# Kernel tuning notes

Hardware: AMD Instinct MI355X
Metric: run time of the kernel (lower is better)

The kernel has to match this reference:

```python
import jax, jax.numpy as jnp
import numpy as np

EMBED_DIM = 1024
NUM_HEADS = 16
D_K = EMBED_DIM // NUM_HEADS
BATCH, SEQ = 4, 2048


def setup_inputs() -> dict:
    key = jax.random.key(0)
    ks = jax.random.split(key, 6)
    s = 1.0 / np.sqrt(EMBED_DIM)
    return {
        "x": jax.random.normal(ks[0], (BATCH, SEQ, EMBED_DIM), dtype=jnp.float32),
        "mask": jnp.ones((BATCH, SEQ), dtype=jnp.int32),
        "Wq": jax.random.uniform(ks[1], (EMBED_DIM, EMBED_DIM), jnp.float32, -s, s),
        "Wk": jax.random.uniform(ks[2], (EMBED_DIM, EMBED_DIM), jnp.float32, -s, s),
        "Wv": jax.random.uniform(ks[3], (EMBED_DIM, EMBED_DIM), jnp.float32, -s, s),
        "Wo": jax.random.uniform(ks[4], (EMBED_DIM, EMBED_DIM), jnp.float32, -s, s),
    }


def reference(x, mask, Wq, Wk, Wv, Wo):
    B, S, E = x.shape
    H, Dk = NUM_HEADS, D_K
    # nn.Linear: y = x @ W.T ; reshape to [B, H, S, Dk]
    def proj(W):
        return jnp.einsum('bse,fe->bsf', x, W).reshape(B, S, H, Dk).transpose(0, 2, 1, 3)
    q, k, v = proj(Wq), proj(Wk), proj(Wv)
    scores = jnp.einsum('bhqd,bhkd->bhqk', q, k) / jnp.sqrt(jnp.float32(Dk))
    # key-padding mask: [B, S] -> [B, 1, 1, S]; 0 means masked with -inf
    scores = jnp.where(mask[:, None, None, :] == 0, -jnp.inf, scores)
    attn = jax.nn.softmax(scores, axis=-1)  # dropout is identity (p=0 / eval)
    out = jnp.einsum('bhqk,bhkd->bhqd', attn, v)
    out = out.transpose(0, 2, 1, 3).reshape(B, S, E)
    return jnp.einsum('bse,fe->bsf', out, Wo)
```

## Files before the change

kernel.cpp:

```cpp
#include <hip/hip_runtime.h>

typedef __attribute__((ext_vector_type(8))) __bf16   bf16x8;
typedef __attribute__((ext_vector_type(8))) _Float16 f16x8;
typedef __attribute__((ext_vector_type(2))) __fp16   h16x2;
typedef __attribute__((ext_vector_type(8))) __fp16   h16x8;
typedef __attribute__((ext_vector_type(4))) float    f32x4;

#define MFMA_BF16 __builtin_amdgcn_mfma_f32_16x16x32_bf16
#define MFMA_F16  __builtin_amdgcn_mfma_f32_16x16x32_f16

__global__ __launch_bounds__(256)
void prep_all(const float* __restrict__ x,  const float* __restrict__ Wq,
              const float* __restrict__ Wk, const float* __restrict__ Wv,
              const float* __restrict__ Wo, const int* __restrict__ mask,
              __bf16* __restrict__ xh, __bf16* __restrict__ w3,
              __bf16* __restrict__ wo, float* __restrict__ bias)
{
    const int i = blockIdx.x * 256 + threadIdx.x;
    const int WSZ8 = 131072;

    if (i < 1572864) {
        const float* src; __bf16* dst; int o8;
        if (i < 1048576)      { src = x;  dst = xh;            o8 = i; }
        else if (i < 1179648) { src = Wq; dst = w3;            o8 = i - 1048576; }
        else if (i < 1310720) { src = Wk; dst = w3 + 1048576;  o8 = i - 1179648; }
        else if (i < 1441792) { src = Wv; dst = w3 + 2097152;  o8 = i - 1310720; }
        else                  { src = Wo; dst = wo;            o8 = i - 1441792; }
        float4 v0 = *(const float4*)(src + (size_t)o8 * 8);
        float4 v1 = *(const float4*)(src + (size_t)o8 * 8 + 4);
        float xs[8] = {v0.x, v0.y, v0.z, v0.w, v1.x, v1.y, v1.z, v1.w};
        bf16x8 h8;
        #pragma unroll
        for (int jj = 0; jj < 8; jj++) h8[jj] = (__bf16)xs[jj];
        *(bf16x8*)(dst + (size_t)o8 * 8) = h8;
    } else {
        int c = i - 1572864;
        int4 m0 = *(const int4*)(mask + c * 8);
        int4 m1 = *(const int4*)(mask + c * 8 + 4);
        float4 b0, b1;
        b0.x = m0.x ? 0.f : -30000.f;  b0.y = m0.y ? 0.f : -30000.f;
        b0.z = m0.z ? 0.f : -30000.f;  b0.w = m0.w ? 0.f : -30000.f;
        b1.x = m1.x ? 0.f : -30000.f;  b1.y = m1.y ? 0.f : -30000.f;
        b1.z = m1.z ? 0.f : -30000.f;  b1.w = m1.w ? 0.f : -30000.f;
        *(float4*)(bias + c * 8)     = b0;
        *(float4*)(bias + c * 8 + 4) = b1;
    }
}

#define GEMM_DECLS                                                          \
    __shared__ __bf16 Ah[128][40], Bh[128][40];                             \
    const int t    = threadIdx.x;                                           \
    const int lane = t & 63;                                                \
    const int wid  = t >> 6;                                                \
    const int l15  = lane & 15;                                             \
    const int lg   = lane >> 4;                                             \
    const int wr   = wid >> 1, wc = wid & 1;

#define GEMM_LOOP(Ag, Bg, m0, brow0, K)                                     \
    f32x4 acc[4][4];                                                        \
    _Pragma("unroll")                                                       \
    for (int i = 0; i < 4; i++)                                             \
        _Pragma("unroll")                                                   \
        for (int jj = 0; jj < 4; jj++)                                      \
            _Pragma("unroll")                                               \
            for (int r = 0; r < 4; r++) acc[i][jj][r] = 0.f;                \
    for (int k0 = 0; k0 < K; k0 += 32) {                                    \
        __syncthreads();                                                    \
        _Pragma("unroll")                                                   \
        for (int i = 0; i < 2; i++) {                                       \
            int id = t + 256 * i;                                           \
            int row = id >> 2, cc = id & 3;                                 \
            *(bf16x8*)&Ah[row][cc*8] =                                      \
                *(const bf16x8*)(Ag + (size_t)(m0 + row) * K + k0 + cc*8);  \
            *(bf16x8*)&Bh[row][cc*8] =                                      \
                *(const bf16x8*)(Bg + (size_t)(brow0 + row) * K + k0 + cc*8);\
        }                                                                   \
        __syncthreads();                                                    \
        bf16x8 ah[4];                                                       \
        _Pragma("unroll")                                                   \
        for (int mr = 0; mr < 4; mr++)                                      \
            ah[mr] = *(const bf16x8*)&Ah[wr*64 + mr*16 + l15][lg*8];        \
        _Pragma("unroll")                                                   \
        for (int nr = 0; nr < 4; nr++) {                                    \
            bf16x8 bh = *(const bf16x8*)&Bh[wc*64 + nr*16 + l15][lg*8];     \
            _Pragma("unroll")                                               \
            for (int mr = 0; mr < 4; mr++)                                  \
                acc[mr][nr] = MFMA_BF16(ah[mr], bh, acc[mr][nr], 0, 0, 0);  \
        }                                                                   \
    }

__global__ __launch_bounds__(256, 4)
void gemm_qkv(const __bf16* __restrict__ xh, const __bf16* __restrict__ w3,
              __bf16* __restrict__ qh, __bf16* __restrict__ kh,
              _Float16* __restrict__ vh)
{
    GEMM_DECLS
    const int K = 1024, N = 1024;
    const int m0     = blockIdx.x * 128;
    const int by     = blockIdx.y;
    const int region = by >> 3;
    const int n0     = (by & 7) * 128;
    const int brow0  = region * 1024 + n0;
    GEMM_LOOP(xh, w3, m0, brow0, K)

    constexpr float QSCALE = 0.18033688011112f;
    #pragma unroll
    for (int mr = 0; mr < 4; mr++)
    #pragma unroll
    for (int r = 0; r < 4; r++) {
        int row = m0 + wr*64 + mr*16 + lg*4 + r;
        #pragma unroll
        for (int nr = 0; nr < 4; nr++) {
            int col = n0 + wc*64 + nr*16 + l15;
            size_t off = (size_t)row * N + col;
            float v = acc[mr][nr][r];
            if (region == 0)      qh[off] = (__bf16)(v * QSCALE);
            else if (region == 1) kh[off] = (__bf16)v;
            else                  vh[off] = (_Float16)v;
        }
    }
}

__global__ __launch_bounds__(256, 4)
void gemm_out(const __bf16* __restrict__ aoh, const __bf16* __restrict__ woh,
              float* __restrict__ out, int M, int N, int K)
{
    GEMM_DECLS
    const int m0 = blockIdx.x * 128, n0 = blockIdx.y * 128;
    GEMM_LOOP(aoh, woh, m0, n0, K)

    #pragma unroll
    for (int mr = 0; mr < 4; mr++)
    #pragma unroll
    for (int r = 0; r < 4; r++) {
        int row = m0 + wr*64 + mr*16 + lg*4 + r;
        #pragma unroll
        for (int nr = 0; nr < 4; nr++) {
            int col = n0 + wc*64 + nr*16 + l15;
            out[(size_t)row * N + col] = acc[mr][nr][r];
        }
    }
}

__global__ __launch_bounds__(512, 2)
void attn_bf16(const __bf16* __restrict__ Qg, const __bf16* __restrict__ Kg,
               const _Float16* __restrict__ Vg, const float* __restrict__ biasg,
               __bf16* AO)
{
    const int S = 2048, E = 1024;
    __shared__ __align__(16) char smem[36864];

    const int tid  = threadIdx.x;
    const int lane = tid & 63;
    const int wid  = tid >> 6;
    const int l15  = lane & 15;
    const int lg   = lane >> 4;

    const int fid = blockIdx.x;
    const int xcd = fid & 7;
    const int j   = fid >> 3;
    const int bh  = xcd * 8 + (j >> 3);
    const int qb  = j & 7;
    const int h   = bh & 15;
    const int b   = bh >> 4;
    const int q0  = qb * 256;
    const size_t base = (size_t)b * S * E + (size_t)h * 64;

    bf16x8 qf[2][2];
    #pragma unroll
    for (int mg = 0; mg < 2; mg++) {
        size_t qoff = base + (size_t)(q0 + wid*32 + mg*16 + l15) * E;
        #pragma unroll
        for (int kc = 0; kc < 2; kc++)
            qf[mg][kc] = *(const bf16x8*)(Qg + qoff + kc*32 + lg*8);
    }

    f32x4 o[2][4], osum[2];
    #pragma unroll
    for (int mg = 0; mg < 2; mg++) {
        #pragma unroll
        for (int nt = 0; nt < 4; nt++)
            #pragma unroll
            for (int r = 0; r < 4; r++) o[mg][nt][r] = 0.f;
        #pragma unroll
        for (int r = 0; r < 4; r++) osum[mg][r] = 0.f;
    }

    f16x8 ones8;
    #pragma unroll
    for (int jj = 0; jj < 8; jj++) ones8[jj] = (_Float16)1.0f;

    const int srow = tid >> 3;
    const int scc  = tid & 7;
    const int sg   = ((srow & 12) >> 2) * 8 + ((srow >> 4) & 1) * 4
                   + (srow & 3) + (srow & 32);

    bf16x8 kpre; f16x8 vpre;
    {
        size_t g0 = base + (size_t)srow * E + scc * 8;
        kpre = *(const bf16x8*)(Kg + g0);
        vpre = *(const f16x8*)(Vg + g0);
    }

    const int NT = S / 64;
    for (int t = 0; t < NT; t++) {
        const int k0 = t * 64;
        char* buf = smem + (t & 1) * 18432;
        __bf16   (*Kh)[72] = (__bf16 (*)[72])buf;
        _Float16 (*Vt)[72] = (_Float16 (*)[72])(buf + 9216);

        *(bf16x8*)&Kh[srow][scc*8] = kpre;
        {
            int colw = (((sg >> 3) ^ scc) << 3) + (sg & 7);
            #pragma unroll
            for (int jj = 0; jj < 8; jj++)
                Vt[scc*8 + jj][colw] = vpre[jj];
        }

        if (t + 1 < NT) {
            size_t gn = base + (size_t)(k0 + 64 + srow) * E + scc * 8;
            kpre = *(const bf16x8*)(Kg + gn);
            vpre = *(const f16x8*)(Vg + gn);
        }
        __syncthreads();

        f32x4 sf[2][4];
        #pragma unroll
        for (int kvb = 0; kvb < 4; kvb++) {
            f32x4 bias4 = *(const f32x4*)(biasg + b * S + k0 + kvb*16 + lg*4);
            sf[0][kvb] = bias4;
            sf[1][kvb] = bias4;
        }
        #pragma unroll
        for (int kc = 0; kc < 2; kc++)
            #pragma unroll
            for (int kvb = 0; kvb < 4; kvb++) {
                bf16x8 kb = *(const bf16x8*)&Kh[kvb*16 + l15][kc*32 + lg*8];
                #pragma unroll
                for (int mg = 0; mg < 2; mg++)
                    sf[mg][kvb] = MFMA_BF16(kb, qf[mg][kc], sf[mg][kvb], 0, 0, 0);
            }

        f16x8 pa[2][2];
        #pragma unroll
        for (int mg = 0; mg < 2; mg++) {
            float p[4][4];
            #pragma unroll
            for (int kvb = 0; kvb < 4; kvb++)
                #pragma unroll
                for (int r = 0; r < 4; r++)
                    p[kvb][r] = __builtin_amdgcn_exp2f(sf[mg][kvb][r]);
            #pragma unroll
            for (int hh = 0; hh < 2; hh++) {
                h16x2 c0 = __builtin_amdgcn_cvt_pkrtz(p[2*hh][0],   p[2*hh][1]);
                h16x2 c1 = __builtin_amdgcn_cvt_pkrtz(p[2*hh][2],   p[2*hh][3]);
                h16x2 c2 = __builtin_amdgcn_cvt_pkrtz(p[2*hh+1][0], p[2*hh+1][1]);
                h16x2 c3 = __builtin_amdgcn_cvt_pkrtz(p[2*hh+1][2], p[2*hh+1][3]);
                h16x8 t8 = __builtin_shufflevector(
                    __builtin_shufflevector(c0, c1, 0, 1, 2, 3),
                    __builtin_shufflevector(c2, c3, 0, 1, 2, 3),
                    0, 1, 2, 3, 4, 5, 6, 7);
                pa[mg][hh] = __builtin_bit_cast(f16x8, t8);
            }
        }

        #pragma unroll
        for (int hh = 0; hh < 2; hh++) {
            #pragma unroll
            for (int nt = 0; nt < 4; nt++) {
                int c8p = (hh*4 + lg) ^ (nt*2 + (l15 >> 3));
                f16x8 vb = *(const f16x8*)&Vt[nt*16 + l15][c8p*8];
                o[0][nt] = MFMA_F16(pa[0][hh], vb, o[0][nt], 0, 0, 0);
                o[1][nt] = MFMA_F16(pa[1][hh], vb, o[1][nt], 0, 0, 0);
            }
            osum[0] = MFMA_F16(pa[0][hh], ones8, osum[0], 0, 0, 0);
            osum[1] = MFMA_F16(pa[1][hh], ones8, osum[1], 0, 0, 0);
        }
    }

    float inv[2][4];
    #pragma unroll
    for (int mg = 0; mg < 2; mg++)
        #pragma unroll
        for (int r = 0; r < 4; r++) inv[mg][r] = 1.0f / osum[mg][r];

    unsigned short* Pu = (unsigned short*)smem;
    __syncthreads();
    #pragma unroll
    for (int mg = 0; mg < 2; mg++)
        #pragma unroll
        for (int r = 0; r < 4; r++)
            #pragma unroll
            for (int nt = 0; nt < 4; nt++) {
                __bf16 v = (__bf16)(o[mg][nt][r] * inv[mg][r]);
                Pu[(wid*32 + mg*16 + lg*4 + r) * 72 + nt*16 + l15] =
                    *(unsigned short*)&v;
            }
    __syncthreads();
    #pragma unroll
    for (int i = 0; i < 4; i++) {
        int u   = tid + 512 * i;
        int row = u >> 3, c8 = u & 7;
        bf16x8 v8;
        #pragma unroll
        for (int jj = 0; jj < 8; jj++) {
            unsigned short us = Pu[row * 72 + c8*8 + jj];
            v8[jj] = *(__bf16*)&us;
        }
        *(bf16x8*)(AO + base + (size_t)(q0 + row) * E + c8 * 8) = v8;
    }
}

extern "C" void kernel_launch(void* const* d_in, const int* in_sizes, int n_in,
                              void* d_out, int out_size, void* d_ws, size_t ws_size,
                              hipStream_t stream)
{
    const float* x    = (const float*)d_in[0];
    const int*   mask = (const int*)  d_in[1];
    const float* Wq   = (const float*)d_in[2];
    const float* Wk   = (const float*)d_in[3];
    const float* Wv   = (const float*)d_in[4];
    const float* Wo   = (const float*)d_in[5];
    float* out = (float*)d_out;

    const int B = 4, S = 2048, E = 1024;
    const int M = B * S;
    const size_t SZ  = (size_t)M * E;
    const size_t WSZ = (size_t)E * E;
    const size_t PB  = SZ * sizeof(__bf16);

    char* ws = (char*)d_ws;
    __bf16*   qh = (__bf16*)(ws);
    __bf16*   kh = (__bf16*)(ws + PB);
    _Float16* vh = (_Float16*)(ws + 2*PB);
    __bf16*   xh = (__bf16*)(ws + 3*PB);
    __bf16*   w3 = (__bf16*)(ws + 4*PB);
    __bf16*   wo = (__bf16*)(ws + 4*PB + 3*WSZ*sizeof(__bf16));
    float*    bs = (float*)(ws + 4*PB + 4*WSZ*sizeof(__bf16));

    prep_all<<<dim3(6148), dim3(256), 0, stream>>>(
        x, Wq, Wk, Wv, Wo, mask, xh, w3, wo, bs);

    gemm_qkv<<<dim3(M/128, 24), dim3(256), 0, stream>>>(xh, w3, qh, kh, vh);

    attn_bf16<<<dim3(512), dim3(512), 0, stream>>>(qh, kh, vh, bs, qh);

    gemm_out<<<dim3(M/128, E/128), dim3(256), 0, stream>>>(qh, wo, out, M, E, E);
}
```

Before: 196.6 us.

## Software-pipeline attention PV with next QK and halve block size

The attention kernel now runs 256-thread blocks over 128-query tiles, launching twice as many blocks, and each thread stages two K/V rows per tile. The main loop is software-pipelined: the PV MFMAs for the previous tile, using the retained probabilities and the previous V buffer, are issued alongside the QK MFMAs of the current tile, with a prologue and an epilogue. The aim is to overlap exp and convert latency with MFMA work and to improve occupancy and load balance. In exchange, each block reloads K/V for fewer queries, which doubles K/V traffic, adds an extra barrier per iteration, and raises register pressure.

```diff
diff --git a/kernel.cpp b/kernel.cpp
--- a/kernel.cpp
+++ b/kernel.cpp
@@ -17,7 +17,6 @@
               __bf16* __restrict__ wo, float* __restrict__ bias)
 {
     const int i = blockIdx.x * 256 + threadIdx.x;
-    const int WSZ8 = 131072;
 
     if (i < 1572864) {
         const float* src; __bf16* dst; int o8;
@@ -142,7 +141,7 @@
     }
 }
 
-__global__ __launch_bounds__(512, 2)
+__global__ __launch_bounds__(256, 2)
 void attn_bf16(const __bf16* __restrict__ Qg, const __bf16* __restrict__ Kg,
                const _Float16* __restrict__ Vg, const float* __restrict__ biasg,
                __bf16* AO)
@@ -159,11 +158,11 @@
     const int fid = blockIdx.x;
     const int xcd = fid & 7;
     const int j   = fid >> 3;
-    const int bh  = xcd * 8 + (j >> 3);
-    const int qb  = j & 7;
+    const int bh  = xcd * 8 + (j >> 4);
+    const int qb  = j & 15;
     const int h   = bh & 15;
     const int b   = bh >> 4;
-    const int q0  = qb * 256;
+    const int q0  = qb * 128;
     const size_t base = (size_t)b * S * E + (size_t)h * 64;
 
     bf16x8 qf[2][2];
@@ -190,46 +189,49 @@
     #pragma unroll
     for (int jj = 0; jj < 8; jj++) ones8[jj] = (_Float16)1.0f;
 
-    const int srow = tid >> 3;
-    const int scc  = tid & 7;
-    const int sg   = ((srow & 12) >> 2) * 8 + ((srow >> 4) & 1) * 4
-                   + (srow & 3) + (srow & 32);
-
-    bf16x8 kpre; f16x8 vpre;
+    const int srow0 = tid >> 3;
+    const int srow1 = srow0 + 32;
+    const int scc   = tid & 7;
+    const int sg0   = ((srow0 & 12) >> 2) * 8 + ((srow0 >> 4) & 1) * 4
+                    + (srow0 & 3) + (srow0 & 32);
+    const int sg1   = ((srow1 & 12) >> 2) * 8 + ((srow1 >> 4) & 1) * 4
+                    + (srow1 & 3) + (srow1 & 32);
+    const int colw0 = (((sg0 >> 3) ^ scc) << 3) + (sg0 & 7);
+    const int colw1 = (((sg1 >> 3) ^ scc) << 3) + (sg1 & 7);
+
+    bf16x8 kpre0, kpre1; f16x8 vpre0, vpre1;
     {
-        size_t g0 = base + (size_t)srow * E + scc * 8;
-        kpre = *(const bf16x8*)(Kg + g0);
-        vpre = *(const f16x8*)(Vg + g0);
+        size_t ga = base + (size_t)srow0 * E + scc * 8;
+        size_t gb = base + (size_t)srow1 * E + scc * 8;
+        kpre0 = *(const bf16x8*)(Kg + ga);  vpre0 = *(const f16x8*)(Vg + ga);
+        kpre1 = *(const bf16x8*)(Kg + gb);  vpre1 = *(const f16x8*)(Vg + gb);
     }
 
     const int NT = S / 64;
-    for (int t = 0; t < NT; t++) {
-        const int k0 = t * 64;
-        char* buf = smem + (t & 1) * 18432;
-        __bf16   (*Kh)[72] = (__bf16 (*)[72])buf;
-        _Float16 (*Vt)[72] = (_Float16 (*)[72])(buf + 9216);
-
-        *(bf16x8*)&Kh[srow][scc*8] = kpre;
+    f16x8 pa_prev[2][2];
+
+    {
+        __bf16   (*Kh)[72] = (__bf16 (*)[72])smem;
+        _Float16 (*Vt)[72] = (_Float16 (*)[72])(smem + 9216);
+        *(bf16x8*)&Kh[srow0][scc*8] = kpre0;
+        *(bf16x8*)&Kh[srow1][scc*8] = kpre1;
+        #pragma unroll
+        for (int jj = 0; jj < 8; jj++) Vt[scc*8 + jj][colw0] = vpre0[jj];
+        #pragma unroll
+        for (int jj = 0; jj < 8; jj++) Vt[scc*8 + jj][colw1] = vpre1[jj];
         {
-            int colw = (((sg >> 3) ^ scc) << 3) + (sg & 7);
-            #pragma unroll
-            for (int jj = 0; jj < 8; jj++)
-                Vt[scc*8 + jj][colw] = vpre[jj];
-        }
-
-        if (t + 1 < NT) {
-            size_t gn = base + (size_t)(k0 + 64 + srow) * E + scc * 8;
-            kpre = *(const bf16x8*)(Kg + gn);
-            vpre = *(const f16x8*)(Vg + gn);
+            size_t ga = base + (size_t)(64 + srow0) * E + scc * 8;
+            size_t gb = base + (size_t)(64 + srow1) * E + scc * 8;
+            kpre0 = *(const bf16x8*)(Kg + ga);  vpre0 = *(const f16x8*)(Vg + ga);
+            kpre1 = *(const bf16x8*)(Kg + gb);  vpre1 = *(const f16x8*)(Vg + gb);
         }
         __syncthreads();
 
         f32x4 sf[2][4];
         #pragma unroll
         for (int kvb = 0; kvb < 4; kvb++) {
-            f32x4 bias4 = *(const f32x4*)(biasg + b * S + k0 + kvb*16 + lg*4);
-            sf[0][kvb] = bias4;
-            sf[1][kvb] = bias4;
+            f32x4 bias4 = *(const f32x4*)(biasg + b * S + kvb*16 + lg*4);
+            sf[0][kvb] = bias4;  sf[1][kvb] = bias4;
         }
         #pragma unroll
         for (int kc = 0; kc < 2; kc++)
@@ -240,8 +242,6 @@
                 for (int mg = 0; mg < 2; mg++)
                     sf[mg][kvb] = MFMA_BF16(kb, qf[mg][kc], sf[mg][kvb], 0, 0, 0);
             }
-
-        f16x8 pa[2][2];
         #pragma unroll
         for (int mg = 0; mg < 2; mg++) {
             float p[4][4];
@@ -260,21 +260,101 @@
                     __builtin_shufflevector(c0, c1, 0, 1, 2, 3),
                     __builtin_shufflevector(c2, c3, 0, 1, 2, 3),
                     0, 1, 2, 3, 4, 5, 6, 7);
-                pa[mg][hh] = __builtin_bit_cast(f16x8, t8);
-            }
-        }
+                pa_prev[mg][hh] = __builtin_bit_cast(f16x8, t8);
+            }
+        }
+    }
+
+    for (int t = 1; t < NT; t++) {
+        const int k0 = t * 64;
+        char* bufc = smem + (t & 1) * 18432;
+        char* bufp = smem + ((t - 1) & 1) * 18432;
+        __bf16   (*Kh)[72]  = (__bf16 (*)[72])bufc;
+        _Float16 (*Vt)[72]  = (_Float16 (*)[72])(bufc + 9216);
+        _Float16 (*Vtp)[72] = (_Float16 (*)[72])(bufp + 9216);
+
+        __syncthreads();
+        *(bf16x8*)&Kh[srow0][scc*8] = kpre0;
+        *(bf16x8*)&Kh[srow1][scc*8] = kpre1;
+        #pragma unroll
+        for (int jj = 0; jj < 8; jj++) Vt[scc*8 + jj][colw0] = vpre0[jj];
+        #pragma unroll
+        for (int jj = 0; jj < 8; jj++) Vt[scc*8 + jj][colw1] = vpre1[jj];
+
+        if (t + 1 < NT) {
+            size_t ga = base + (size_t)(k0 + 64 + srow0) * E + scc * 8;
+            size_t gb = base + (size_t)(k0 + 64 + srow1) * E + scc * 8;
+            kpre0 = *(const bf16x8*)(Kg + ga);  vpre0 = *(const f16x8*)(Vg + ga);
+            kpre1 = *(const bf16x8*)(Kg + gb);  vpre1 = *(const f16x8*)(Vg + gb);
+        }
+        __syncthreads();
+
+        f32x4 sf[2][4];
+        #pragma unroll
+        for (int kvb = 0; kvb < 4; kvb++) {
+            f32x4 bias4 = *(const f32x4*)(biasg + b * S + k0 + kvb*16 + lg*4);
+            sf[0][kvb] = bias4;  sf[1][kvb] = bias4;
+        }
+        #pragma unroll
+        for (int kc = 0; kc < 2; kc++)
+            #pragma unroll
+            for (int kvb = 0; kvb < 4; kvb++) {
+                bf16x8 kb = *(const bf16x8*)&Kh[kvb*16 + l15][kc*32 + lg*8];
+                #pragma unroll
+                for (int mg = 0; mg < 2; mg++)
+                    sf[mg][kvb] = MFMA_BF16(kb, qf[mg][kc], sf[mg][kvb], 0, 0, 0);
+            }
 
         #pragma unroll
         for (int hh = 0; hh < 2; hh++) {
             #pragma unroll
             for (int nt = 0; nt < 4; nt++) {
                 int c8p = (hh*4 + lg) ^ (nt*2 + (l15 >> 3));
-                f16x8 vb = *(const f16x8*)&Vt[nt*16 + l15][c8p*8];
-                o[0][nt] = MFMA_F16(pa[0][hh], vb, o[0][nt], 0, 0, 0);
-                o[1][nt] = MFMA_F16(pa[1][hh], vb, o[1][nt], 0, 0, 0);
-            }
-            osum[0] = MFMA_F16(pa[0][hh], ones8, osum[0], 0, 0, 0);
-            osum[1] = MFMA_F16(pa[1][hh], ones8, osum[1], 0, 0, 0);
+                f16x8 vb = *(const f16x8*)&Vtp[nt*16 + l15][c8p*8];
+                o[0][nt] = MFMA_F16(pa_prev[0][hh], vb, o[0][nt], 0, 0, 0);
+                o[1][nt] = MFMA_F16(pa_prev[1][hh], vb, o[1][nt], 0, 0, 0);
+            }
+            osum[0] = MFMA_F16(pa_prev[0][hh], ones8, osum[0], 0, 0, 0);
+            osum[1] = MFMA_F16(pa_prev[1][hh], ones8, osum[1], 0, 0, 0);
+        }
+
+        #pragma unroll
+        for (int mg = 0; mg < 2; mg++) {
+            float p[4][4];
+            #pragma unroll
+            for (int kvb = 0; kvb < 4; kvb++)
+                #pragma unroll
+                for (int r = 0; r < 4; r++)
+                    p[kvb][r] = __builtin_amdgcn_exp2f(sf[mg][kvb][r]);
+            #pragma unroll
+            for (int hh = 0; hh < 2; hh++) {
+                h16x2 c0 = __builtin_amdgcn_cvt_pkrtz(p[2*hh][0],   p[2*hh][1]);
+                h16x2 c1 = __builtin_amdgcn_cvt_pkrtz(p[2*hh][2],   p[2*hh][3]);
+                h16x2 c2 = __builtin_amdgcn_cvt_pkrtz(p[2*hh+1][0], p[2*hh+1][1]);
+                h16x2 c3 = __builtin_amdgcn_cvt_pkrtz(p[2*hh+1][2], p[2*hh+1][3]);
+                h16x8 t8 = __builtin_shufflevector(
+                    __builtin_shufflevector(c0, c1, 0, 1, 2, 3),
+                    __builtin_shufflevector(c2, c3, 0, 1, 2, 3),
+                    0, 1, 2, 3, 4, 5, 6, 7);
+                pa_prev[mg][hh] = __builtin_bit_cast(f16x8, t8);
+            }
+        }
+    }
+
+    {
+        char* bufp = smem + ((NT - 1) & 1) * 18432;
+        _Float16 (*Vtp)[72] = (_Float16 (*)[72])(bufp + 9216);
+        #pragma unroll
+        for (int hh = 0; hh < 2; hh++) {
+            #pragma unroll
+            for (int nt = 0; nt < 4; nt++) {
+                int c8p = (hh*4 + lg) ^ (nt*2 + (l15 >> 3));
+                f16x8 vb = *(const f16x8*)&Vtp[nt*16 + l15][c8p*8];
+                o[0][nt] = MFMA_F16(pa_prev[0][hh], vb, o[0][nt], 0, 0, 0);
+                o[1][nt] = MFMA_F16(pa_prev[1][hh], vb, o[1][nt], 0, 0, 0);
+            }
+            osum[0] = MFMA_F16(pa_prev[0][hh], ones8, osum[0], 0, 0, 0);
+            osum[1] = MFMA_F16(pa_prev[1][hh], ones8, osum[1], 0, 0, 0);
         }
     }
 
@@ -299,7 +379,7 @@
     __syncthreads();
     #pragma unroll
     for (int i = 0; i < 4; i++) {
-        int u   = tid + 512 * i;
+        int u   = tid + 256 * i;
         int row = u >> 3, c8 = u & 7;
         bf16x8 v8;
         #pragma unroll
@@ -343,7 +423,7 @@
 
     gemm_qkv<<<dim3(M/128, 24), dim3(256), 0, stream>>>(xh, w3, qh, kh, vh);
 
-    attn_bf16<<<dim3(512), dim3(512), 0, stream>>>(qh, kh, vh, bs, qh);
+    attn_bf16<<<dim3(1024), dim3(256), 0, stream>>>(qh, kh, vh, bs, qh);
 
     gemm_out<<<dim3(M/128, E/128), dim3(256), 0, stream>>>(qh, wo, out, M, E, E);
 }
```

Result: no change. 197.8 us (median of 3 runs) (+0.6%).

## Load K fragments directly from global, shrink attention blocks to 128 queries

Applied to the files above, without the earlier changes.

The attention kernel now reads K operand fragments for the QK MFMA straight from global memory into registers, prefetching the next tile, instead of staging K through LDS. LDS holds only a single-buffered transposed V tile, with a sync at the top of each iteration. Blocks shrink to 256 threads and 128 query rows, launching 1024 blocks instead of 512. This cuts LDS traffic and footprint and may raise occupancy, but each block now fetches K redundantly from global/L2 and the single-buffered V adds a barrier per iteration.

```diff
diff --git a/kernel.cpp b/kernel.cpp
--- a/kernel.cpp
+++ b/kernel.cpp
@@ -17,7 +17,6 @@
               __bf16* __restrict__ wo, float* __restrict__ bias)
 {
     const int i = blockIdx.x * 256 + threadIdx.x;
-    const int WSZ8 = 131072;
 
     if (i < 1572864) {
         const float* src; __bf16* dst; int o8;
@@ -142,13 +141,14 @@
     }
 }
 
-__global__ __launch_bounds__(512, 2)
+__global__ __launch_bounds__(256, 2)
 void attn_bf16(const __bf16* __restrict__ Qg, const __bf16* __restrict__ Kg,
                const _Float16* __restrict__ Vg, const float* __restrict__ biasg,
                __bf16* AO)
 {
     const int S = 2048, E = 1024;
-    __shared__ __align__(16) char smem[36864];
+    __shared__ __align__(16) char smem[18432];
+    _Float16 (*Vt)[72] = (_Float16 (*)[72])smem;
 
     const int tid  = threadIdx.x;
     const int lane = tid & 63;
@@ -159,11 +159,11 @@
     const int fid = blockIdx.x;
     const int xcd = fid & 7;
     const int j   = fid >> 3;
-    const int bh  = xcd * 8 + (j >> 3);
-    const int qb  = j & 7;
+    const int bh  = xcd * 8 + (j >> 4);
+    const int qb  = j & 15;
     const int h   = bh & 15;
     const int b   = bh >> 4;
-    const int q0  = qb * 256;
+    const int q0  = qb * 128;
     const size_t base = (size_t)b * S * E + (size_t)h * 64;
 
     bf16x8 qf[2][2];
@@ -190,37 +190,49 @@
     #pragma unroll
     for (int jj = 0; jj < 8; jj++) ones8[jj] = (_Float16)1.0f;
 
-    const int srow = tid >> 3;
-    const int scc  = tid & 7;
-    const int sg   = ((srow & 12) >> 2) * 8 + ((srow >> 4) & 1) * 4
-                   + (srow & 3) + (srow & 32);
-
-    bf16x8 kpre; f16x8 vpre;
+    const int srow0 = tid >> 3;
+    const int srow1 = srow0 + 32;
+    const int scc   = tid & 7;
+    const int sg0   = ((srow0 & 12) >> 2) * 8 + ((srow0 >> 4) & 1) * 4
+                    + (srow0 & 3) + (srow0 & 32);
+    const int sg1   = ((srow1 & 12) >> 2) * 8 + ((srow1 >> 4) & 1) * 4
+                    + (srow1 & 3) + (srow1 & 32);
+    const int colw0 = (((sg0 >> 3) ^ scc) << 3) + (sg0 & 7);
+    const int colw1 = (((sg1 >> 3) ^ scc) << 3) + (sg1 & 7);
+
+    const __bf16* kbase = Kg + base + (size_t)l15 * E + lg * 8;
+
+    f16x8 vpre0, vpre1;
     {
-        size_t g0 = base + (size_t)srow * E + scc * 8;
-        kpre = *(const bf16x8*)(Kg + g0);
-        vpre = *(const f16x8*)(Vg + g0);
-    }
+        size_t ga = base + (size_t)srow0 * E + scc * 8;
+        size_t gb = base + (size_t)srow1 * E + scc * 8;
+        vpre0 = *(const f16x8*)(Vg + ga);
+        vpre1 = *(const f16x8*)(Vg + gb);
+    }
+    bf16x8 kf[2][4];
+    #pragma unroll
+    for (int kc = 0; kc < 2; kc++)
+        #pragma unroll
+        for (int kvb = 0; kvb < 4; kvb++)
+            kf[kc][kvb] = *(const bf16x8*)(kbase + (size_t)(kvb*16) * E + kc*32);
 
     const int NT = S / 64;
     for (int t = 0; t < NT; t++) {
         const int k0 = t * 64;
-        char* buf = smem + (t & 1) * 18432;
-        __bf16   (*Kh)[72] = (__bf16 (*)[72])buf;
-        _Float16 (*Vt)[72] = (_Float16 (*)[72])(buf + 9216);
-
-        *(bf16x8*)&Kh[srow][scc*8] = kpre;
+        const int tn = (t + 1 < NT) ? t + 1 : t;
+
+        __syncthreads();
+
+        #pragma unroll
+        for (int jj = 0; jj < 8; jj++) Vt[scc*8 + jj][colw0] = vpre0[jj];
+        #pragma unroll
+        for (int jj = 0; jj < 8; jj++) Vt[scc*8 + jj][colw1] = vpre1[jj];
+
         {
-            int colw = (((sg >> 3) ^ scc) << 3) + (sg & 7);
-            #pragma unroll
-            for (int jj = 0; jj < 8; jj++)
-                Vt[scc*8 + jj][colw] = vpre[jj];
-        }
-
-        if (t + 1 < NT) {
-            size_t gn = base + (size_t)(k0 + 64 + srow) * E + scc * 8;
-            kpre = *(const bf16x8*)(Kg + gn);
-            vpre = *(const f16x8*)(Vg + gn);
+            size_t ga = base + (size_t)(tn*64 + srow0) * E + scc * 8;
+            size_t gb = base + (size_t)(tn*64 + srow1) * E + scc * 8;
+            vpre0 = *(const f16x8*)(Vg + ga);
+            vpre1 = *(const f16x8*)(Vg + gb);
         }
         __syncthreads();
 
@@ -228,18 +240,24 @@
         #pragma unroll
         for (int kvb = 0; kvb < 4; kvb++) {
             f32x4 bias4 = *(const f32x4*)(biasg + b * S + k0 + kvb*16 + lg*4);
-            sf[0][kvb] = bias4;
-            sf[1][kvb] = bias4;
+            sf[0][kvb] = bias4;  sf[1][kvb] = bias4;
         }
         #pragma unroll
         for (int kc = 0; kc < 2; kc++)
             #pragma unroll
             for (int kvb = 0; kvb < 4; kvb++) {
-                bf16x8 kb = *(const bf16x8*)&Kh[kvb*16 + l15][kc*32 + lg*8];
                 #pragma unroll
                 for (int mg = 0; mg < 2; mg++)
-                    sf[mg][kvb] = MFMA_BF16(kb, qf[mg][kc], sf[mg][kvb], 0, 0, 0);
+                    sf[mg][kvb] = MFMA_BF16(kf[kc][kvb], qf[mg][kc],
+                                            sf[mg][kvb], 0, 0, 0);
             }
+
+        #pragma unroll
+        for (int kc = 0; kc < 2; kc++)
+            #pragma unroll
+            for (int kvb = 0; kvb < 4; kvb++)
+                kf[kc][kvb] = *(const bf16x8*)(kbase
+                    + (size_t)(tn*64 + kvb*16) * E + kc*32);
 
         f16x8 pa[2][2];
         #pragma unroll
@@ -299,7 +317,7 @@
     __syncthreads();
     #pragma unroll
     for (int i = 0; i < 4; i++) {
-        int u   = tid + 512 * i;
+        int u   = tid + 256 * i;
         int row = u >> 3, c8 = u & 7;
         bf16x8 v8;
         #pragma unroll
@@ -343,7 +361,7 @@
 
     gemm_qkv<<<dim3(M/128, 24), dim3(256), 0, stream>>>(xh, w3, qh, kh, vh);
 
-    attn_bf16<<<dim3(512), dim3(512), 0, stream>>>(qh, kh, vh, bs, qh);
+    attn_bf16<<<dim3(1024), dim3(256), 0, stream>>>(qh, kh, vh, bs, qh);
 
     gemm_out<<<dim3(M/128, E/128), dim3(256), 0, stream>>>(qh, wo, out, M, E, E);
 }
```

New measurement: 291.7 us. +48.4%, slower.
